# Kernel tuning notes

Measured on AMD Instinct MI355X. Metric: run time of the kernel, lower is better.

## Reference

```python
import jax, jax.numpy as jnp
import numpy as np

EPS = 1e-5

def _bn(x, gamma, beta):
    # training-mode BatchNorm2d over (B, H, W) per channel, biased variance
    m = x.mean(axis=(0, 2, 3), keepdims=True)
    v = x.var(axis=(0, 2, 3), keepdims=True)
    return (x - m) * jax.lax.rsqrt(v + EPS) * gamma[None, :, None, None] + beta[None, :, None, None]

@jax.custom_vjp
def _atan_spike(x):
    # Heaviside forward, ATan surrogate (alpha=2) backward
    return (x >= 0.0).astype(x.dtype)

def _atan_fwd(x):
    return _atan_spike(x), x

def _atan_bwd(x, g):
    return (g / (1.0 + (jnp.pi * x) ** 2),)

_atan_spike.defvjp(_atan_fwd, _atan_bwd)

def setup_inputs() -> dict:
    key = jax.random.key(0)
    ks = jax.random.split(key, 3)
    T, N, Cin, Cout, H, W = 4, 8, 512, 256, 32, 32
    x = jax.random.normal(ks[0], (T, N, Cin, H, W), dtype=jnp.float32)
    bn1_gamma = jnp.ones((Cin,), jnp.float32)
    bn1_beta = jnp.zeros((Cin,), jnp.float32)
    conv_w = jax.random.normal(ks[1], (Cout, Cin, 1, 1), jnp.float32) / np.float32(np.sqrt(Cin))
    lif_w = jnp.zeros((1,), jnp.float32)  # sigmoid(0)=0.5 <=> init_tau=2.0
    bn2_gamma = jnp.ones((Cout,), jnp.float32)
    bn2_beta = jnp.zeros((Cout,), jnp.float32)
    up_w = jax.random.normal(ks[2], (Cout, Cout, 4, 4), jnp.float32) / np.float32(np.sqrt(Cout * 16))
    return {"x": x, "bn1_gamma": bn1_gamma, "bn1_beta": bn1_beta, "conv_w": conv_w,
            "lif_w": lif_w, "bn2_gamma": bn2_gamma, "bn2_beta": bn2_beta, "up_w": up_w}

def reference(x, bn1_gamma, bn1_beta, conv_w, lif_w, bn2_gamma, bn2_beta, up_w):
    T, N, Cin, H, W = x.shape
    Cout = conv_w.shape[0]
    # bottleneck: SeqToANNContainer(BN(Cin), Conv2d 1x1 Cin->Cout, no bias)
    xf = x.reshape(T * N, Cin, H, W)
    h = _bn(xf, bn1_gamma, bn1_beta)
    h = jnp.einsum('bchw,oc->bohw', h, conv_w[:, :, 0, 0])
    h = h.reshape(T, N, Cout, H, W)
    # MultiStepParametricLIFNode: v += (x - v)*sigmoid(w); hard reset to 0, detach_reset
    tau_inv = jax.nn.sigmoid(lif_w[0])
    def step(v, xt):
        v = v + (xt - v) * tau_inv
        s = _atan_spike(v - 1.0)
        v = v * (1.0 - jax.lax.stop_gradient(s))
        return v, s
    _, spikes = jax.lax.scan(step, jnp.zeros_like(h[0]), h)
    s = spikes.reshape(T * N, Cout, H, W)
    # ConstantDilation2d(dilation=2): zero-insertion -> (2H-1, 2W-1)
    d = jnp.zeros((T * N, Cout, 2 * H - 1, 2 * W - 1), s.dtype).at[:, :, ::2, ::2].set(s)
    # ConstantPad2d(kernel-1-padding = 4-1-1 = 2)
    d = jnp.pad(d, ((0, 0), (0, 0), (2, 2), (2, 2)))
    d = _bn(d, bn2_gamma, bn2_beta)
    # ConvTranspose2d(k=4, stride=1, padding=3) == VALID conv with channel-swapped, flipped kernel
    kern = up_w.transpose(1, 0, 2, 3)[:, :, ::-1, ::-1]
    out = jax.lax.conv_general_dilated(d, kern, (1, 1), 'VALID',
                                       dimension_numbers=('NCHW', 'OIHW', 'NCHW'))
    return out.reshape(T, N, Cout, 2 * H, 2 * W)
```

## Files before the change

### kernel.cpp

```cpp
#include <hip/hip_runtime.h>
#include <math.h>

#define CIN 512
#define COUT 256
#define TT 4
#define NN 8
#define HH 32
#define WW 32
#define FR (TT*NN)
#define HW (HH*WW)
#define BN_EPS 1e-5
#define FLAGCAP (1<<19)
#define N2 143648.0

typedef unsigned short ushort_t;
typedef unsigned int uint_t;
typedef __attribute__((ext_vector_type(8))) short short8;
typedef __attribute__((ext_vector_type(4))) float f32x4;
typedef __attribute__((ext_vector_type(4))) uint_t u32x4;

__device__ inline ushort_t f2bf(float f) {
    uint_t u = __float_as_uint(f);
    uint_t r = u + 0x7FFFu + ((u >> 16) & 1u);
    return (ushort_t)(r >> 16);
}
__device__ inline float bf2f(ushort_t a) { return __uint_as_float(((uint_t)a) << 16); }

__global__ __launch_bounds__(256) void k_xsplit(const float* __restrict__ x,
                                                ushort_t* __restrict__ Xa_g,
                                                ushort_t* __restrict__ Xb_g,
                                                float* __restrict__ X2_g,
                                                double* __restrict__ bn_s1,
                                                double* __restrict__ bn_s2) {
    int blk = blockIdx.x;
    int n = blk >> 6;
    int hw0 = (blk & 63) << 4;
    int tid = threadIdx.x;
    int pg = tid & 3;
    int rr = tid >> 2;

    __shared__ ushort_t La[8192];
    __shared__ ushort_t Lb[8192];
    __shared__ float X2s[64];

    float x2loc[16];
    float s1v[8], s2v[8];
#pragma unroll
    for (int q = 0; q < 16; ++q) x2loc[q] = 0.f;
#pragma unroll
    for (int q = 0; q < 8; ++q) { s1v[q] = 0.f; s2v[q] = 0.f; }
    if (tid < 64) X2s[tid] = 0.f;

#pragma unroll
    for (int kc = 0; kc < 4; ++kc) {
        int c0 = kc << 7;
        __syncthreads();
#pragma unroll
        for (int sw = 0; sw < 8; ++sw) {
            const int t = sw >> 1;
            int i = ((sw & 1) << 6) + rr;
            const float4 v = *reinterpret_cast<const float4*>(
                &x[(((size_t)((t * NN + n) * CIN) + c0 + i) << 10) + hw0 + (pg << 2)]);
            int cbl = i >> 3, e = i & 7;
            int slot = (kc << 1) + (sw & 1);
#pragma unroll
            for (int k = 0; k < 4; ++k) {
                float xv = (k == 0) ? v.x : (k == 1) ? v.y : (k == 2) ? v.z : v.w;
                ushort_t a = f2bf(xv);
                ushort_t b = f2bf(xv - bf2f(a));
                x2loc[(k << 2) + t] += xv * xv;
                s1v[slot] += xv;
                s2v[slot] += xv * xv;
                int lrx = (k << 2) + t;
                uint_t u = ((((uint_t)(pg * 16 + cbl)) * 16 + lrx) << 3) + e;
                uint_t byteoff = (u << 1) ^ ((uint_t)pg << 5);
                *(ushort_t*)((char*)La + byteoff) = a;
                *(ushort_t*)((char*)Lb + byteoff) = b;
            }
        }
        __syncthreads();
        for (int q = tid; q < 1024; q += 256) {
            int pg2 = q >> 8;
            uint_t lo = (uint_t)(q & 255) << 4;
            uint_t src = (((uint_t)pg2 << 12) + lo) ^ ((uint_t)pg2 << 5);
            u32x4 va = *(u32x4*)((char*)La + src);
            u32x4 vb = *(u32x4*)((char*)Lb + src);
            size_t dst = (((size_t)blk * 4 + pg2) << 13) + ((size_t)kc << 11) + ((size_t)(q & 255) << 3);
            __builtin_nontemporal_store(va, (u32x4*)(Xa_g + dst));
            __builtin_nontemporal_store(vb, (u32x4*)(Xb_g + dst));
        }
    }
#pragma unroll
    for (int slot = 0; slot < 8; ++slot) {
        float a1 = s1v[slot], a2v = s2v[slot];
        a1 += __shfl_xor(a1, 1); a1 += __shfl_xor(a1, 2);
        a2v += __shfl_xor(a2v, 1); a2v += __shfl_xor(a2v, 2);
        if (pg == 0) {
            int c = ((slot >> 1) << 7) + ((slot & 1) << 6) + rr;
            atomicAdd(&bn_s1[c], (double)a1);
            atomicAdd(&bn_s2[c], (double)a2v);
        }
    }
    __syncthreads();
#pragma unroll
    for (int k = 0; k < 4; ++k)
#pragma unroll
        for (int t = 0; t < 4; ++t)
            atomicAdd(&X2s[pg * 16 + k * 4 + t], x2loc[(k << 2) + t]);
    __syncthreads();
    if (tid < 64) X2_g[(blk << 6) + tid] = X2s[tid];
}

__global__ __launch_bounds__(512) void k_bn1_fin(const double* __restrict__ bn_s1,
                                                 const double* __restrict__ bn_s2,
                                                 const float* __restrict__ gamma1,
                                                 double* __restrict__ mean,
                                                 double* __restrict__ alpha) {
    int c = threadIdx.x;
    double n = (double)(FR * HW);
    double m = bn_s1[c] / n;
    double var = bn_s2[c] / n - m * m;
    mean[c] = m;
    alpha[c] = (double)gamma1[c] / sqrt(var + BN_EPS);
}

__global__ __launch_bounds__(256) void k_prep_wsplit(const float* __restrict__ conv_w,
                                                     const float* __restrict__ beta1,
                                                     const double* __restrict__ mean,
                                                     const double* __restrict__ alpha,
                                                     double* __restrict__ w2t,
                                                     ushort_t* __restrict__ Wa,
                                                     ushort_t* __restrict__ Wb,
                                                     float* __restrict__ W2,
                                                     double* __restrict__ bias) {
    int o = blockIdx.x;
    float s2 = 0.f;
    double sb = 0.0;
    for (int c = threadIdx.x; c < CIN; c += 256) {
        double cw = (double)conv_w[(size_t)o * CIN + c];
        double w = cw * alpha[c];
        w2t[(size_t)c * COUT + o] = w;
        float wf = (float)w;
        ushort_t a = f2bf(wf);
        ushort_t b = f2bf(wf - bf2f(a));
        size_t base = ((size_t)(c >> 3) * COUT + o) * 8 + (c & 7);
        Wa[base] = a; Wb[base] = b;
        s2 += wf * wf;
        sb += ((double)beta1[c] - mean[c] * alpha[c]) * cw;
    }
    __shared__ float red[256];
    __shared__ double redd[256];
    red[threadIdx.x] = s2;
    redd[threadIdx.x] = sb;
    __syncthreads();
    for (int ofs = 128; ofs > 0; ofs >>= 1) {
        if (threadIdx.x < ofs) {
            red[threadIdx.x] += red[threadIdx.x + ofs];
            redd[threadIdx.x] += redd[threadIdx.x + ofs];
        }
        __syncthreads();
    }
    if (threadIdx.x == 0) { W2[o] = red[0]; bias[o] = redd[0]; }
}

__global__ __launch_bounds__(256) void k_gemm_lif_mfma(
    const ushort_t* __restrict__ Xa_g, const ushort_t* __restrict__ Xb_g,
    const ushort_t* __restrict__ Wa, const ushort_t* __restrict__ Wb,
    const float* __restrict__ X2_g, const float* __restrict__ W2,
    const double* __restrict__ bias, const float* __restrict__ lif_w,
    ushort_t* __restrict__ spk, int* __restrict__ cnt,
    uint_t* __restrict__ flags, uint_t* __restrict__ flagcnt)
{
    int blk = blockIdx.x;
    int n   = blk >> 6;
    int hw0 = (blk & 63) << 4;
    int tid = threadIdx.x;
    int wv = tid >> 6, lane = tid & 63;
    int lr = lane & 15, kq = lane >> 4;
    int pxh = wv >> 1, oh = wv & 1;

    __shared__ uint_t cl[4 * 64 * 8];

    f32x4 acc[2][8];
#pragma unroll
    for (int m = 0; m < 2; ++m)
#pragma unroll
        for (int ot = 0; ot < 8; ++ot) acc[m][ot] = (f32x4){0.f, 0.f, 0.f, 0.f};

    const ushort_t* xa0 = Xa_g + (((size_t)blk) << 15) + ((size_t)pxh << 14) + ((uint_t)lane << 3);
    const ushort_t* xb0 = Xb_g + (((size_t)blk) << 15) + ((size_t)pxh << 14) + ((uint_t)lane << 3);
    const ushort_t* wbase_a = Wa + ((uint_t)kq << 11) + ((uint_t)oh << 10) + ((uint_t)lr << 3);
    const ushort_t* wbase_b = Wb + ((uint_t)kq << 11) + ((uint_t)oh << 10) + ((uint_t)lr << 3);

#pragma unroll 2
    for (int ks = 0; ks < 16; ++ks) {
        short8 fa0 = *(const short8*)(xa0 + (ks << 9));
        short8 fa1 = *(const short8*)(xa0 + 8192 + (ks << 9));
        short8 fb0 = *(const short8*)(xb0 + (ks << 9));
        short8 fb1 = *(const short8*)(xb0 + 8192 + (ks << 9));
        const ushort_t* wpa = wbase_a + (ks << 13);
        const ushort_t* wpb = wbase_b + (ks << 13);
#pragma unroll
        for (int ot = 0; ot < 8; ++ot) {
            short8 wa8 = *(const short8*)(wpa + (ot << 7));
            short8 wb8 = *(const short8*)(wpb + (ot << 7));
            acc[0][ot] = __builtin_amdgcn_mfma_f32_16x16x32_bf16(fa0, wa8, acc[0][ot], 0, 0, 0);
            acc[1][ot] = __builtin_amdgcn_mfma_f32_16x16x32_bf16(fa1, wa8, acc[1][ot], 0, 0, 0);
            acc[0][ot] = __builtin_amdgcn_mfma_f32_16x16x32_bf16(fb0, wa8, acc[0][ot], 0, 0, 0);
            acc[1][ot] = __builtin_amdgcn_mfma_f32_16x16x32_bf16(fb1, wa8, acc[1][ot], 0, 0, 0);
            acc[0][ot] = __builtin_amdgcn_mfma_f32_16x16x32_bf16(fa0, wb8, acc[0][ot], 0, 0, 0);
            acc[1][ot] = __builtin_amdgcn_mfma_f32_16x16x32_bf16(fa1, wb8, acc[1][ot], 0, 0, 0);
        }
    }

    float xs2[2][4];
#pragma unroll
    for (int m = 0; m < 2; ++m)
#pragma unroll
        for (int t = 0; t < 4; ++t)
            xs2[m][t] = X2_g[(blk << 6) + (((pxh << 1) + m) << 4) + (kq << 2) + t];

    for (int q = tid; q < 4 * 64 * 8; q += 256) cl[q] = 0;
    __syncthreads();

    float tauf = (float)(1.0 / (1.0 + exp(-(double)lif_w[0])));
#pragma unroll
    for (int ot = 0; ot < 8; ++ot) {
        int o = (oh << 7) + (ot << 4) + lr;
        float bi = (float)bias[o];
        float w2v = W2[o];
        uint_t cloc = 0;
#pragma unroll
        for (int m = 0; m < 2; ++m) {
            int hw = hw0 + (pxh << 3) + (m << 2) + kq;
            float v = 0.f;
            bool fl = false;
#pragma unroll
            for (int t = 0; t < 4; ++t) {
                float h = acc[m][ot][t] + bi;
                float eps = 4e-5f * sqrtf(w2v * xs2[m][t]) + 5e-5f;
                v += (h - v) * tauf;
                if (fabsf(v - 1.f) <= 2.f * eps) fl = true;
                bool s = (v >= 1.f);
                spk[((size_t)((t * NN + n) * HW) + hw) * COUT + o] = s ? (ushort_t)0x3F80 : (ushort_t)0;
                cloc += s ? 1u : 0u;
                if (s) v = 0.f;
            }
            if (fl) {
                uint_t id = atomicAdd(flagcnt, 1u);
                if (id < FLAGCAP) flags[id] = (((uint_t)(n * HW + hw)) << 8) | (uint_t)o;
            }
        }
        cl[(wv << 9) + (lane << 3) + ot] = cloc;
    }
    __syncthreads();
    {
        int o = tid;
        int ohh = o >> 7, ott = (o >> 4) & 7, lr2 = o & 15;
        uint_t s = 0;
#pragma unroll
        for (int w2 = ohh; w2 < 4; w2 += 2)
#pragma unroll
            for (int k2 = 0; k2 < 4; ++k2)
                s += cl[(w2 << 9) + (((k2 << 4) + lr2) << 3) + ott];
        if (s) atomicAdd(&cnt[o], (int)s);
    }
}

__global__ __launch_bounds__(256) void k_fixup(
    const float* __restrict__ x, const double* __restrict__ w2t,
    const double* __restrict__ bias, const float* __restrict__ lif_w,
    const uint_t* __restrict__ flags, const uint_t* __restrict__ flagcnt,
    ushort_t* __restrict__ spk, int* __restrict__ cnt)
{
    int nf = (int)*flagcnt; if (nf > FLAGCAP) nf = FLAGCAP;
    int wid = (blockIdx.x << 2) + (threadIdx.x >> 6);
    int lane = threadIdx.x & 63;
    double tau = 1.0 / (1.0 + exp(-(double)lif_w[0]));
    for (int g = wid; g < nf; g += 8192) {
        uint_t f = flags[g];
        int o = f & 255;
        int s = f >> 8;
        int n = s >> 10, hw = s & 1023;
        const float* xb = x + ((size_t)n << 19) + hw;
        double p0 = 0.0, p1 = 0.0, p2 = 0.0, p3 = 0.0;
#pragma unroll
        for (int i = 0; i < 8; ++i) {
            int c = lane + (i << 6);
            double wv = w2t[((size_t)c << 8) + o];
            size_t xo = (size_t)c << 10;
            p0 += wv * (double)xb[xo];
            p1 += wv * (double)xb[xo + (1ull << 22)];
            p2 += wv * (double)xb[xo + (2ull << 22)];
            p3 += wv * (double)xb[xo + (3ull << 22)];
        }
#pragma unroll
        for (int ofs = 32; ofs > 0; ofs >>= 1) {
            p0 += __shfl_down(p0, ofs);
            p1 += __shfl_down(p1, ofs);
            p2 += __shfl_down(p2, ofs);
            p3 += __shfl_down(p3, ofs);
        }
        if (lane == 0) {
            double bi = bias[o];
            double hh[4] = {p0 + bi, p1 + bi, p2 + bi, p3 + bi};
            double v = 0.0; int delta = 0;
#pragma unroll
            for (int t = 0; t < 4; ++t) {
                v += (hh[t] - v) * tau;
                bool sn = (v >= 1.0);
                size_t idx = (((size_t)t << 13) + ((size_t)n << 10) + (size_t)hw) * COUT + o;
                ushort_t old = spk[idx];
                ushort_t nw = sn ? (ushort_t)0x3F80 : (ushort_t)0;
                if (old != nw) { spk[idx] = nw; delta += sn ? 1 : -1; }
                if (sn) v = 0.0;
            }
            if (delta) atomicAdd(&cnt[o], delta);
        }
    }
}

__global__ __launch_bounds__(256) void k_wt_prep(const float* __restrict__ up_w,
                                                 const int* __restrict__ cnt,
                                                 const float* __restrict__ gamma2,
                                                 ushort_t* __restrict__ Wt) {
    int blk = blockIdx.x;
    int ij = blk >> 5, cb = blk & 31;
    int o = threadIdx.x;
    __shared__ double a2s[8];
    if (o < 8) {
        int c = (cb << 3) + o;
        double m = (double)cnt[c] / N2;
        a2s[o] = (double)gamma2[c] / sqrt(m - m * m + BN_EPS);
    }
    __syncthreads();
    short8 v;
#pragma unroll
    for (int e = 0; e < 8; ++e) {
        int c = (cb << 3) + e;
        float w = (float)(a2s[e] * (double)up_w[(((size_t)c * COUT) + o) * 16 + ij]);
        v[e] = (short)f2bf(w);
    }
    *(short8*)(Wt + ((size_t)ij << 16) + ((size_t)cb << 11) + ((size_t)o << 3)) = v;
}

__global__ __launch_bounds__(256) void k_kconst(const float* __restrict__ up_w,
                                                const int* __restrict__ cnt,
                                                const float* __restrict__ gamma2,
                                                const float* __restrict__ beta2,
                                                float* __restrict__ kc) {
    int o = blockIdx.x, c = threadIdx.x;
    double m = (double)cnt[c] / N2;
    double a = (double)gamma2[c] / sqrt(m - m * m + BN_EPS);
    double b2v = (double)beta2[c] - m * a;
    const float* u = up_w + ((size_t)c * COUT + o) * 16;
    double t = 0.0;
#pragma unroll
    for (int k = 0; k < 16; ++k) t += (double)u[k];
    double s = b2v * t;
    __shared__ double red[256];
    red[c] = s;
    __syncthreads();
    for (int ofs = 128; ofs > 0; ofs >>= 1) {
        if (c < ofs) red[c] += red[c + ofs];
        __syncthreads();
    }
    if (c == 0) kc[o] = (float)red[0];
}

__global__ __launch_bounds__(512) void k_deconv_mfma(const ushort_t* __restrict__ spk,
                                                     const ushort_t* __restrict__ Wt,
                                                     const float* __restrict__ kc,
                                                     float* __restrict__ out) {
    int p = blockIdx.x;
    int w = ((p & 7) << 7) + (p >> 3);
    int b  = w >> 5;
    int py = (w >> 4) & 1;
    int Yb = (w & 15) << 1;
    int tid = threadIdx.x;
    int wv  = tid >> 6;
    int lane = tid & 63;
    int px = wv >> 2;
    int og = wv & 3;
    int lr = lane & 15;
    int kq = lane >> 4;

    __shared__ __align__(16) char smem[52224];
    ushort_t* slab = (ushort_t*)smem;

    int sb = Yb - 1 + py;
    for (int q = tid; q < 3 * 34 * 32; q += 512) {
        int pix = q >> 5;
        int l = q & 31;
        int r = pix / 34;
        int xc = pix - r * 34;
        int sy = sb + r;
        int sx = xc - 1;
        uint_t off = ((uint_t)(pix << 9) + (uint_t)(l << 4)) ^ ((uint_t)(xc & 7) << 4);
        uint4* dst = (uint4*)((char*)slab + off);
        if (sy >= 0 && sy < 32 && sx >= 0 && sx < 32) {
            *dst = *(const uint4*)(spk + ((size_t)b * HW + sy * 32 + sx) * COUT + l * 8);
        } else {
            *dst = make_uint4(0u, 0u, 0u, 0u);
        }
    }
    __syncthreads();

    f32x4 acc[4][4];
#pragma unroll
    for (int pf = 0; pf < 4; ++pf)
#pragma unroll
        for (int of = 0; of < 4; ++of)
            acc[pf][of] = (f32x4){0.f, 0.f, 0.f, 0.f};

    int obase = og << 6;

#pragma unroll
    for (int dy = 0; dy < 2; ++dy) {
#pragma unroll
        for (int dx = 0; dx < 2; ++dx) {
            int i = 3 - py - 2 * dy;
            int j = 3 - px - 2 * dx;
            const ushort_t* wpij = Wt + ((size_t)(i * 4 + j) << 16);
            uint_t sbase[4], swz[4];
#pragma unroll
            for (int pf = 0; pf < 4; ++pf) {
                int pid = pf * 16 + lr;
                int Yq = pid >> 5;
                int X  = pid & 31;
                int xc = X + dx + px;
                int prow = (Yq + dy) * 34 + xc;
                sbase[pf] = ((uint_t)prow << 9) + ((uint_t)kq << 4);
                swz[pf]   = ((uint_t)(xc & 7)) << 4;
            }
#pragma unroll
            for (int cs = 0; cs < 8; ++cs) {
                short8 aw[4];
#pragma unroll
                for (int of = 0; of < 4; ++of)
                    aw[of] = *(const short8*)(wpij +
                        ((size_t)((cs << 2) + kq) * COUT + obase + (of << 4) + lr) * 8);
                short8 bs[4];
#pragma unroll
                for (int pf = 0; pf < 4; ++pf)
                    bs[pf] = *(const short8*)((const char*)slab +
                              ((sbase[pf] + ((uint_t)cs << 6)) ^ swz[pf]));
#pragma unroll
                for (int pf = 0; pf < 4; ++pf)
#pragma unroll
                    for (int of = 0; of < 4; ++of)
                        acc[pf][of] = __builtin_amdgcn_mfma_f32_16x16x32_bf16(
                            aw[of], bs[pf], acc[pf][of], 0, 0, 0);
            }
        }
    }

    __syncthreads();
    float* stage = (float*)smem;
#pragma unroll 1
    for (int of = 0; of < 4; ++of) {
        if (of) __syncthreads();
#pragma unroll
        for (int rg = 0; rg < 4; ++rg) {
            int row = (og << 4) + (kq << 2) + rg;
#pragma unroll
            for (int pf = 0; pf < 4; ++pf) {
                int Yq = pf >> 1;
                int x = ((((pf & 1) << 4) + lr) << 1) + px;
                uint_t a4 = ((uint_t)row << 5) + ((uint_t)Yq << 4)
                          + (((uint_t)x >> 2) ^ ((uint_t)kq << 2));
                stage[(a4 << 2) + (x & 3)] = acc[pf][of][rg];
            }
        }
        __syncthreads();
#pragma unroll
        for (int rep = 0; rep < 4; ++rep) {
            int u = tid + (rep << 9);
            int r = u >> 5, rem = u & 31;
            int yq = rem >> 4, f4 = rem & 15;
            uint_t a4 = ((uint_t)r << 5) + ((uint_t)yq << 4)
                      + ((uint_t)f4 ^ ((((uint_t)r >> 2) & 3) << 2));
            f32x4 v = ((const f32x4*)stage)[a4];
            int o = ((r >> 4) << 6) + (of << 4) + (r & 15);
            float base = kc[o];
            v[0] += base; v[1] += base; v[2] += base; v[3] += base;
            int y = ((Yb + yq) << 1) + py;
            __builtin_nontemporal_store(v,
                (f32x4*)(out + ((size_t)(b * COUT + o) << 12) + (y << 6) + (f4 << 2)));
        }
    }
}

extern "C" void kernel_launch(void* const* d_in, const int* in_sizes, int n_in,
                              void* d_out, int out_size, void* d_ws, size_t ws_size,
                              hipStream_t stream) {
    (void)in_sizes; (void)n_in; (void)out_size; (void)ws_size;
    const float* x        = (const float*)d_in[0];
    const float* bn1_g    = (const float*)d_in[1];
    const float* bn1_b    = (const float*)d_in[2];
    const float* conv_w   = (const float*)d_in[3];
    const float* lif_w    = (const float*)d_in[4];
    const float* bn2_g    = (const float*)d_in[5];
    const float* bn2_b    = (const float*)d_in[6];
    const float* up_w     = (const float*)d_in[7];
    float* out = (float*)d_out;

    char* ws = (char*)d_ws;
    ushort_t* spk  = (ushort_t*)(ws + 0);
    ushort_t* Xa_g = (ushort_t*)(ws + 16777216);
    ushort_t* Xb_g = (ushort_t*)(ws + 50331648);
    float*  X2_g   = (float*)  (ws + 83886080);
    float*  W2     = (float*)  (ws + 84017152);
    double* mean   = (double*) (ws + 84018176);
    double* alpha  = (double*) (ws + 84022272);
    double* w2t    = (double*) (ws + 84026368);
    double* bias   = (double*) (ws + 85074944);
    int*    cnt    = (int*)    (ws + 85081088);
    float*  kc     = (float*)  (ws + 85082112);
    ushort_t* Wt   = (ushort_t*)(ws + 85083136);
    ushort_t* Wa   = (ushort_t*)(ws + 87180288);
    ushort_t* Wb   = (ushort_t*)(ws + 87442432);
    uint_t* flagcnt= (uint_t*) (ws + 87704576);
    uint_t* flags  = (uint_t*) (ws + 87705600);
    double* bn_s1  = (double*) (ws + 89802752);
    double* bn_s2  = (double*) (ws + 89806848);

    hipMemsetAsync(cnt, 0, COUT * sizeof(int), stream);
    hipMemsetAsync(flagcnt, 0, sizeof(uint_t), stream);
    hipMemsetAsync(bn_s1, 0, 2 * CIN * sizeof(double), stream);

    k_xsplit<<<512, 256, 0, stream>>>(x, Xa_g, Xb_g, X2_g, bn_s1, bn_s2);
    k_bn1_fin<<<1, 512, 0, stream>>>(bn_s1, bn_s2, bn1_g, mean, alpha);
    k_prep_wsplit<<<COUT, 256, 0, stream>>>(conv_w, bn1_b, mean, alpha, w2t, Wa, Wb, W2, bias);
    k_gemm_lif_mfma<<<512, 256, 0, stream>>>(Xa_g, Xb_g, Wa, Wb, X2_g, W2,
                                             bias, lif_w, spk, cnt, flags, flagcnt);
    k_fixup<<<2048, 256, 0, stream>>>(x, w2t, bias, lif_w, flags, flagcnt, spk, cnt);
    k_wt_prep<<<512, 256, 0, stream>>>(up_w, cnt, bn2_g, Wt);
    k_kconst<<<COUT, 256, 0, stream>>>(up_w, cnt, bn2_g, bn2_b, kc);
    k_deconv_mfma<<<32 * 2 * 16, 512, 0, stream>>>(spk, Wt, kc, out);
}
```

Measured before the change: 434.0 us.

## Move BN1 statistics into a dedicated reduction kernel and drop memsets

Replaces the double-precision atomic accumulation of BN1 sums inside k_xsplit plus the single-block finalize kernel with a separate per-channel reduction kernel that reads x once more and computes mean/alpha directly. The three hipMemsetAsync calls are replaced by a tiny init kernel. The deconv output store also switches from nontemporal to regular float4 stores. This removes contended fp64 atomics and memset launches, at the cost of an extra full pass over the 64 MB input.

```diff
diff --git a/kernel.cpp b/kernel.cpp
--- a/kernel.cpp
+++ b/kernel.cpp
@@ -26,12 +26,47 @@
 }
 __device__ inline float bf2f(ushort_t a) { return __uint_as_float(((uint_t)a) << 16); }
 
+__global__ __launch_bounds__(256) void k_init(int* __restrict__ cnt,
+                                              uint_t* __restrict__ flagcnt) {
+    int t = threadIdx.x;
+    cnt[t] = 0;
+    if (t == 0) *flagcnt = 0u;
+}
+
+__global__ __launch_bounds__(256) void k_bn1_stats(const float* __restrict__ x,
+                                                   const float* __restrict__ gamma1,
+                                                   double* __restrict__ mean,
+                                                   double* __restrict__ alpha) {
+    int c = blockIdx.x;
+    int tid = threadIdx.x;
+    double s1 = 0.0, s2 = 0.0;
+    const float4* x4 = reinterpret_cast<const float4*>(x);
+    for (int f = 0; f < FR; ++f) {
+        size_t base4 = ((size_t)(f * CIN + c) * HW) >> 2;
+        float4 v = x4[base4 + tid];
+        s1 += (double)v.x + (double)v.y + (double)v.z + (double)v.w;
+        s2 += (double)v.x * v.x + (double)v.y * v.y + (double)v.z * v.z + (double)v.w * v.w;
+    }
+    __shared__ double l1[256], l2[256];
+    l1[tid] = s1; l2[tid] = s2;
+    __syncthreads();
+    for (int ofs = 128; ofs > 0; ofs >>= 1) {
+        if (tid < ofs) { l1[tid] += l1[tid + ofs]; l2[tid] += l2[tid + ofs]; }
+        __syncthreads();
+    }
+    if (tid == 0) {
+        double n = (double)(FR * HW);
+        double m = l1[0] / n;
+        double var = l2[0] / n - m * m;
+        mean[c] = m;
+        alpha[c] = (double)gamma1[c] / sqrt(var + BN_EPS);
+    }
+}
+
 __global__ __launch_bounds__(256) void k_xsplit(const float* __restrict__ x,
                                                 ushort_t* __restrict__ Xa_g,
                                                 ushort_t* __restrict__ Xb_g,
-                                                float* __restrict__ X2_g,
-                                                double* __restrict__ bn_s1,
-                                                double* __restrict__ bn_s2) {
+                                                float* __restrict__ X2_g) {
     int blk = blockIdx.x;
     int n = blk >> 6;
     int hw0 = (blk & 63) << 4;
@@ -44,11 +79,8 @@
     __shared__ float X2s[64];
 
     float x2loc[16];
-    float s1v[8], s2v[8];
 #pragma unroll
     for (int q = 0; q < 16; ++q) x2loc[q] = 0.f;
-#pragma unroll
-    for (int q = 0; q < 8; ++q) { s1v[q] = 0.f; s2v[q] = 0.f; }
     if (tid < 64) X2s[tid] = 0.f;
 
 #pragma unroll
@@ -62,15 +94,12 @@
             const float4 v = *reinterpret_cast<const float4*>(
                 &x[(((size_t)((t * NN + n) * CIN) + c0 + i) << 10) + hw0 + (pg << 2)]);
             int cbl = i >> 3, e = i & 7;
-            int slot = (kc << 1) + (sw & 1);
 #pragma unroll
             for (int k = 0; k < 4; ++k) {
                 float xv = (k == 0) ? v.x : (k == 1) ? v.y : (k == 2) ? v.z : v.w;
                 ushort_t a = f2bf(xv);
                 ushort_t b = f2bf(xv - bf2f(a));
                 x2loc[(k << 2) + t] += xv * xv;
-                s1v[slot] += xv;
-                s2v[slot] += xv * xv;
                 int lrx = (k << 2) + t;
                 uint_t u = ((((uint_t)(pg * 16 + cbl)) * 16 + lrx) << 3) + e;
                 uint_t byteoff = (u << 1) ^ ((uint_t)pg << 5);
@@ -90,17 +119,6 @@
             __builtin_nontemporal_store(vb, (u32x4*)(Xb_g + dst));
         }
     }
-#pragma unroll
-    for (int slot = 0; slot < 8; ++slot) {
-        float a1 = s1v[slot], a2v = s2v[slot];
-        a1 += __shfl_xor(a1, 1); a1 += __shfl_xor(a1, 2);
-        a2v += __shfl_xor(a2v, 1); a2v += __shfl_xor(a2v, 2);
-        if (pg == 0) {
-            int c = ((slot >> 1) << 7) + ((slot & 1) << 6) + rr;
-            atomicAdd(&bn_s1[c], (double)a1);
-            atomicAdd(&bn_s2[c], (double)a2v);
-        }
-    }
     __syncthreads();
 #pragma unroll
     for (int k = 0; k < 4; ++k)
@@ -109,19 +127,6 @@
             atomicAdd(&X2s[pg * 16 + k * 4 + t], x2loc[(k << 2) + t]);
     __syncthreads();
     if (tid < 64) X2_g[(blk << 6) + tid] = X2s[tid];
-}
-
-__global__ __launch_bounds__(512) void k_bn1_fin(const double* __restrict__ bn_s1,
-                                                 const double* __restrict__ bn_s2,
-                                                 const float* __restrict__ gamma1,
-                                                 double* __restrict__ mean,
-                                                 double* __restrict__ alpha) {
-    int c = threadIdx.x;
-    double n = (double)(FR * HW);
-    double m = bn_s1[c] / n;
-    double var = bn_s2[c] / n - m * m;
-    mean[c] = m;
-    alpha[c] = (double)gamma1[c] / sqrt(var + BN_EPS);
 }
 
 __global__ __launch_bounds__(256) void k_prep_wsplit(const float* __restrict__ conv_w,
@@ -480,13 +485,12 @@
             int yq = rem >> 4, f4 = rem & 15;
             uint_t a4 = ((uint_t)r << 5) + ((uint_t)yq << 4)
                       + ((uint_t)f4 ^ ((((uint_t)r >> 2) & 3) << 2));
-            f32x4 v = ((const f32x4*)stage)[a4];
+            float4 v = ((const float4*)stage)[a4];
             int o = ((r >> 4) << 6) + (of << 4) + (r & 15);
             float base = kc[o];
-            v[0] += base; v[1] += base; v[2] += base; v[3] += base;
+            v.x += base; v.y += base; v.z += base; v.w += base;
             int y = ((Yb + yq) << 1) + py;
-            __builtin_nontemporal_store(v,
-                (f32x4*)(out + ((size_t)(b * COUT + o) << 12) + (y << 6) + (f4 << 2)));
+            *(float4*)(out + ((size_t)(b * COUT + o) << 12) + (y << 6) + (f4 << 2)) = v;
         }
     }
 }
@@ -522,15 +526,10 @@
     ushort_t* Wb   = (ushort_t*)(ws + 87442432);
     uint_t* flagcnt= (uint_t*) (ws + 87704576);
     uint_t* flags  = (uint_t*) (ws + 87705600);
-    double* bn_s1  = (double*) (ws + 89802752);
-    double* bn_s2  = (double*) (ws + 89806848);
-
-    hipMemsetAsync(cnt, 0, COUT * sizeof(int), stream);
-    hipMemsetAsync(flagcnt, 0, sizeof(uint_t), stream);
-    hipMemsetAsync(bn_s1, 0, 2 * CIN * sizeof(double), stream);
-
-    k_xsplit<<<512, 256, 0, stream>>>(x, Xa_g, Xb_g, X2_g, bn_s1, bn_s2);
-    k_bn1_fin<<<1, 512, 0, stream>>>(bn_s1, bn_s2, bn1_g, mean, alpha);
+
+    k_init<<<1, 256, 0, stream>>>(cnt, flagcnt);
+    k_bn1_stats<<<CIN, 256, 0, stream>>>(x, bn1_g, mean, alpha);
+    k_xsplit<<<512, 256, 0, stream>>>(x, Xa_g, Xb_g, X2_g);
     k_prep_wsplit<<<COUT, 256, 0, stream>>>(conv_w, bn1_b, mean, alpha, w2t, Wa, Wb, W2, bias);
     k_gemm_lif_mfma<<<512, 256, 0, stream>>>(Xa_g, Xb_g, Wa, Wb, X2_g, W2,
                                              bias, lif_w, spk, cnt, flags, flagcnt);
```

Measured after the change: 443.5 us. 2.2% more time.
